# Performance work log

Measured on AMD Instinct MI355X. Metric: run time of the kernel, lower is better.

## Reference

```python
import jax, jax.numpy as jnp
import numpy as np
from jax import lax

EPS = 1e-5

# Straight-through identity binarization (torch code mutates .data, so autograd
# sees binarized values but grads flow as identity to the latent weights/inputs).
def ste_sign(x):
    return x + lax.stop_gradient(jnp.sign(x) - x)

# SignActivation: sign forward, hard-tanh-style gradient (zero where |i| > 1).
@jax.custom_vjp
def sign_act(x):
    return jnp.sign(x)

def _sa_fwd(x):
    return jnp.sign(x), x

def _sa_bwd(x, g):
    return (jnp.where(jnp.abs(x) <= 1.0, g, 0.0),)

sign_act.defvjp(_sa_fwd, _sa_bwd)

def bn2d(x, gamma, beta):
    # training-mode BatchNorm2d: batch stats over (N,H,W), biased variance
    mean = jnp.mean(x, axis=(0, 2, 3), keepdims=True)
    var = jnp.var(x, axis=(0, 2, 3), keepdims=True)
    xn = (x - mean) * lax.rsqrt(var + EPS)
    return xn * gamma.reshape(1, -1, 1, 1) + beta.reshape(1, -1, 1, 1)

def bn1d(x, gamma, beta):
    mean = jnp.mean(x, axis=0, keepdims=True)
    var = jnp.var(x, axis=0, keepdims=True)
    xn = (x - mean) * lax.rsqrt(var + EPS)
    return xn * gamma[None, :] + beta[None, :]

def conv2d(x, w, stride, pad):
    return lax.conv_general_dilated(
        x, w, window_strides=(stride, stride),
        padding=((pad, pad), (pad, pad)),
        dimension_numbers=("NCHW", "OIHW", "NCHW"))


def setup_inputs() -> dict:
    key = jax.random.key(0)
    ks = jax.random.split(key, 4)
    width = 0.01
    x = jax.random.normal(ks[0], (8192, 1, 28, 28), dtype=jnp.float32)
    w1 = jax.random.normal(ks[1], (32, 1, 5, 5), dtype=jnp.float32) * width
    w2 = jax.random.normal(ks[2], (64, 32, 4, 4), dtype=jnp.float32) * width
    w3 = jax.random.normal(ks[3], (10, 64 * 64), dtype=jnp.float32) * width
    g1 = jnp.ones((32,), jnp.float32); b1 = jnp.zeros((32,), jnp.float32)
    g2 = jnp.ones((64,), jnp.float32); b2 = jnp.zeros((64,), jnp.float32)
    g3 = jnp.ones((10,), jnp.float32); b3 = jnp.zeros((10,), jnp.float32)
    return {"x": x, "w1": w1, "g1": g1, "b1": b1,
            "w2": w2, "g2": g2, "b2": b2,
            "w3": w3, "g3": g3, "b3": b3}


def reference(x, w1, g1, b1, w2, g2, b2, w3, g3, b3):
    # cv1: input channels = 1 != 3 -> input binarized; weight binarized
    h = conv2d(ste_sign(x), ste_sign(w1), stride=2, pad=2)   # [B,32,14,14]
    h = bn2d(h, g1, b1)
    h = sign_act(h)
    # cv2: input channels 32 != 3 -> binarized (no-op on +-1 values)
    h = conv2d(ste_sign(h), ste_sign(w2), stride=2, pad=2)   # [B,64,8,8]
    h = bn2d(h, g2, b2)
    h = sign_act(h)
    h = h.reshape(h.shape[0], -1)                            # [B,4096]
    # fc3: features 4096 != 784 -> binarized (no-op on +-1 values)
    h = jnp.dot(ste_sign(h), ste_sign(w3).T)                 # [B,10]
    h = bn1d(h, g3, b3)
    return h
```

## Files before the change

kernel.cpp:

```cpp
#include <hip/hip_runtime.h>
#include <stdint.h>


#define NB 8192
typedef unsigned long long ull;

#define OFF_C1  ((size_t)0)
#define SZ_C1   ((size_t)NB*6272)
#define OFF_C2  (OFF_C1 + SZ_C1)
#define SZ_C2   ((size_t)NB*4096)
#define OFF_FC  (OFF_C2 + SZ_C2)
#define SZ_FC   ((size_t)NB*10*4)
#define OFF_S1  (OFF_FC + SZ_FC)
#define OFF_S2  (OFF_S1 + 2048)
#define OFF_S3  (OFF_S2 + 8192)
#define OFF_W2B (OFF_S3 + 2048)
#define OFF_W3B (OFF_W2B + 4096)

__device__ inline void mk_thresh(double s, double t, int &T, int &flip) {
    if (s > 0.0) {
        int v = (int)floor(-t / s) - 2;
        for (int c = 0; c < 6; ++c) { if (s * (double)v + t > 0.0) break; ++v; }
        T = v; flip = 0;
    } else if (s < 0.0) {
        int v = (int)floor(-t / s) - 2;
        for (int c = 0; c < 6; ++c) { if (!(s * (double)v + t > 0.0)) break; ++v; }
        T = v; flip = 1;
    } else { T = -200; flip = (t > 0.0) ? 0 : 1; }
}
__device__ inline int clampT(int T, int lim) {
    return (T < -lim) ? -lim : (T > lim) ? lim : T;
}

__global__ __launch_bounds__(256) void kA_conv1(
    const float* __restrict__ x, const float* __restrict__ w1,
    const float* __restrict__ w2, const float* __restrict__ w3,
    int8_t* __restrict__ c1out, int* __restrict__ stats1,
    ull* __restrict__ w2bT, ull* __restrict__ w3b)
{
    const int tid = threadIdx.x, lane = tid & 63, wv = tid >> 6;

    if (blockIdx.x == 2048) {
        for (int m = wv; m < 10; m += 4) {
            const float* wp = w3 + (size_t)m*4096;
            ull mine = 0ull;
            for (int ch = 0; ch < 64; ++ch) {
                const ull bal = __ballot(wp[(size_t)ch*64 + lane] > 0.f);
                if (lane == ch) mine = bal;
            }
            w3b[m*64 + lane] = mine;
        }
        for (int t = tid; t < 512; t += 256) {
            const int idx = t >> 6, k = t & 63;
            const int u = idx >> 1, pr = idx & 1;
            uint32_t lo = 0u, hi = 0u;
            for (int c = 0; c < 32; ++c) {
                const float* wp = w2 + (((k*32 + c)*4 + u)*4 + 2*pr);
                lo |= (wp[0] > 0.f ? 1u : 0u) << c;
                hi |= (wp[1] > 0.f ? 1u : 0u) << c;
            }
            w2bT[t] = (ull)lo | ((ull)hi << 32);
        }
        return;
    }

    __shared__ ull sxb[4][16];
    __shared__ uint32_t wfilt[32];
    __shared__ uint32_t outb[4][1568];
    __shared__ int lsum[32], lsq[32];

    if (tid < 32) {
        uint32_t f = 0u;
        #pragma unroll
        for (int q = 0; q < 25; ++q) f |= (w1[tid*25 + q] > 0.f ? 1u : 0u) << q;
        wfilt[tid] = f;
        lsum[tid] = 0; lsq[tid] = 0;
    }
    const int n = blockIdx.x*4 + wv;
    #pragma unroll
    for (int t = 0; t < 13; ++t) {
        const int idx = t*64 + lane;
        const float v = (idx < 784) ? x[(size_t)n*784 + idx] : -1.f;
        const ull bal = __ballot(v > 0.f);
        if (lane == t) sxb[wv][t] = bal;
    }
    if (lane == 13) sxb[wv][13] = 0ull;
    __syncthreads();
    for (int t = 0; t < 4; ++t) {
        const int p = t*64 + lane;
        if (p < 196) {
            const int i = p / 14, j = p - i*14;
            const uint32_t cmask = (j == 0) ? 0x1Cu : (j == 13) ? 0x0Fu : 0x1Fu;
            uint32_t win = 0u, vm = 0u;
            #pragma unroll
            for (int u = 0; u < 5; ++u) {
                const int r = 2*i + u - 2;
                if (r >= 0 && r < 28) {
                    const int bp = 28*r, w0 = bp >> 6, sh = bp & 63;
                    const ull a = sxb[wv][w0], b = sxb[wv][w0+1];
                    uint32_t row = (uint32_t)((a >> sh) | ((b << 1) << (63 - sh)));
                    row = (row & 0x0FFFFFFFu) << 2;
                    win |= ((row >> (2*j)) & 31u) << (5*u);
                    vm  |= cmask << (5*u);
                }
            }
            const int nv = __popc(vm);
            uint32_t dw[8];
            #pragma unroll
            for (int d = 0; d < 8; ++d) dw[d] = 0u;
            #pragma unroll
            for (int c = 0; c < 32; ++c) {
                const int diff = __popc((win ^ wfilt[c]) & vm);
                const int o = nv - 2*diff;
                dw[c >> 2] |= (uint32_t)(o & 255) << (8*(c & 3));
            }
            #pragma unroll
            for (int d = 0; d < 8; ++d) outb[wv][p*8 + d] = dw[d];
        }
    }
    __syncthreads();
    {
        int4* dst = (int4*)(c1out + (size_t)n*6272);
        const int4* src = (const int4*)&outb[wv][0];
        #pragma unroll
        for (int t = 0; t < 7; ++t) {
            const int idx = t*64 + lane;
            if (idx < 392) dst[idx] = src[idx];
        }
    }
    {
        const int ch = lane & 31, half = lane >> 5;
        const int8_t* ob = (const int8_t*)&outb[wv][0];
        int s = 0, q = 0;
        for (int p = half*98; p < half*98 + 98; ++p) {
            const int v = ob[p*32 + ch];
            s += v; q += v*v;
        }
        s += __shfl_xor(s, 32);
        q += __shfl_xor(q, 32);
        if (lane < 32) { atomicAdd(&lsum[lane], s); atomicAdd(&lsq[lane], q); }
    }
    __syncthreads();
    if (tid < 32) {
        const int shard = blockIdx.x & 7;
        atomicAdd(&stats1[(shard*32 + tid)*2 + 0], lsum[tid]);
        atomicAdd(&stats1[(shard*32 + tid)*2 + 1], lsq[tid]);
    }
}

__global__ __launch_bounds__(256) void kB_conv2(
    const int8_t* __restrict__ c1out, const int* __restrict__ stats1,
    const float* __restrict__ gm1, const float* __restrict__ bt1,
    const ull* __restrict__ w2bT,
    int8_t* __restrict__ c2out, ull* __restrict__ stats2)
{
    __shared__ ull BwU[4][14][8];
    __shared__ ull sW[512];
    __shared__ int sT1[32];
    __shared__ uint32_t sFlip1;
    __shared__ uint32_t cw[4][64][16];
    __shared__ int ssum[64], ssq[64];
    const int tid = threadIdx.x, lane = tid & 63, wv = tid >> 6;
    const int n0 = blockIdx.x * 4;

    for (int t = tid; t < 512; t += 256) sW[t] = w2bT[t];
    if (tid < 64) { ssum[tid] = 0; ssq[tid] = 0; }
    if (tid < 32) {
        long long s = 0, q = 0;
        for (int sh = 0; sh < 8; ++sh) {
            s += stats1[(sh*32 + tid)*2 + 0];
            q += stats1[(sh*32 + tid)*2 + 1];
        }
        const double N = 8192.0 * 196.0;
        const double mean = (double)s / N;
        const double var  = (double)q / N - mean*mean;
        const double a = (double)gm1[tid] / sqrt(var + 1e-5);
        const double b = (double)bt1[tid] - mean*a;
        int T, fl; mk_thresh(a, b, T, fl);
        sT1[tid] = clampT(T, 26);
        const ull bm = __ballot(fl != 0);
        if (tid == 0) sFlip1 = (uint32_t)bm;
    }
    __syncthreads();
    const uint32_t flipn1 = ~sFlip1;
    for (int t = tid; t < 784; t += 256) {
        const int im = t / 196, p = t - im*196;
        const int r = p / 14, c = p - r*14;
        const uint4* src = (const uint4*)(c1out + ((size_t)(n0+im)*196 + p)*32);
        const uint4 lo4 = src[0], hi4 = src[1];
        const uint32_t wsrc[8] = {lo4.x, lo4.y, lo4.z, lo4.w, hi4.x, hi4.y, hi4.z, hi4.w};
        uint32_t neg = 0u;
        #pragma unroll
        for (int d = 0; d < 8; ++d) {
            #pragma unroll
            for (int qq = 0; qq < 4; ++qq) {
                const int ch = d*4 + qq;
                const int v = (int)((int8_t)(wsrc[d] >> (8*qq)));
                neg |= ((uint32_t)(v - sT1[ch]) >> 31) << ch;
            }
        }
        ((uint32_t*)&BwU[im][r][0])[c] = neg ^ flipn1;
    }
    __syncthreads();
    ull W[8];
    #pragma unroll
    for (int idx = 0; idx < 8; ++idx) W[idx] = sW[idx*64 + lane];
    int s = 0, q = 0;
    #pragma unroll
    for (int i = 0; i < 8; ++i) {
        uint32_t packA = 0u;
        #pragma unroll
        for (int j = 0; j < 8; ++j) {
            int D = 0, nw = 0;
            #pragma unroll
            for (int u = 0; u < 4; ++u) {
                const int r = 2*i + u - 2;
                if (r < 0 || r > 13) continue;
                const ull* row = &BwU[wv][r][0];
                if (j >= 1) { D += __popcll(row[j-1] ^ W[2*u+0]); ++nw; }
                if (j <= 6) { D += __popcll(row[j]   ^ W[2*u+1]); ++nw; }
            }
            const int o = 32*nw - D;
            s += o; q += o*o;
            packA |= (uint32_t)(o & 255) << (8*(j & 3));
            if ((j & 3) == 3) { cw[wv][lane][2*i + (j >> 2)] = packA; packA = 0u; }
        }
    }
    atomicAdd(&ssum[lane], s);
    atomicAdd(&ssq[lane], q);
    __syncthreads();
    {
        const int n = n0 + wv;
        int4* dst = (int4*)(c2out + (size_t)n*4096);
        const int4* src = (const int4*)&cw[wv][0][0];
        #pragma unroll
        for (int t = 0; t < 4; ++t) dst[t*64 + lane] = src[t*64 + lane];
    }
    if (tid < 64) {
        const int shard = blockIdx.x & 7;
        atomicAdd(&stats2[(shard*64 + tid)*2 + 0], (ull)(long long)ssum[tid]);
        atomicAdd(&stats2[(shard*64 + tid)*2 + 1], (ull)(long long)ssq[tid]);
    }
}

__global__ __launch_bounds__(256) void kC_fc(
    const int8_t* __restrict__ c2o, const float* __restrict__ gm2,
    const float* __restrict__ bt2, const ull* __restrict__ stats2,
    const ull* __restrict__ w3b,
    int* __restrict__ fc, ull* __restrict__ stats3)
{
    __shared__ ull w3s[640];
    __shared__ int sT2[64];
    __shared__ ull sFlip2;
    __shared__ int fco[4][10];
    __shared__ int s3[10], q3[10];
    const int tid = threadIdx.x, lane = tid & 63, wv = tid >> 6;
    for (int t = tid; t < 640; t += 256) w3s[t] = w3b[t];
    if (tid < 10) { s3[tid] = 0; q3[tid] = 0; }
    if (tid < 64) {
        long long ss = 0, qq = 0;
        for (int sh = 0; sh < 8; ++sh) {
            ss += (long long)stats2[(sh*64 + tid)*2 + 0];
            qq += (long long)stats2[(sh*64 + tid)*2 + 1];
        }
        const double N = 8192.0 * 64.0;
        const double mh = (double)ss / N;
        const double vh = (double)qq / N - mh*mh;
        const double a = (double)gm2[tid] / sqrt(4.0*vh + 1e-5);
        const double b = (double)bt2[tid] - 2.0*mh*a;
        int T, fl; mk_thresh(2.0*a, b, T, fl);
        sT2[tid] = clampT(T, 200);
        const ull bm = __ballot(fl != 0);
        if (tid == 0) sFlip2 = bm;
    }
    __syncthreads();
    const int T2 = sT2[lane];
    const ull flipn2 = ~sFlip2;
    const int n = blockIdx.x*4 + wv;
    const uint4* src = (const uint4*)(c2o + (size_t)n*4096 + lane*64);
    uint32_t neglo = 0u, neghi = 0u;
    #pragma unroll
    for (int r4 = 0; r4 < 4; ++r4) {
        const uint4 v4 = src[r4];
        const uint32_t wsrc[4] = {v4.x, v4.y, v4.z, v4.w};
        #pragma unroll
        for (int c = 0; c < 4; ++c) {
            #pragma unroll
            for (int b = 0; b < 4; ++b) {
                const int p = r4*16 + c*4 + b;
                const int v = (int)((int8_t)(wsrc[c] >> (8*b)));
                const uint32_t bit = (uint32_t)(v - T2) >> 31;
                if (p < 32) neglo |= bit << p; else neghi |= bit << (p - 32);
            }
        }
    }
    const ull myw = ((ull)neglo | ((ull)neghi << 32)) ^ flipn2;
    uint32_t pk[5];
    #pragma unroll
    for (int t = 0; t < 5; ++t) {
        const uint32_t pa = (uint32_t)__popcll(myw ^ w3s[(2*t+0)*64 + lane]);
        const uint32_t pb = (uint32_t)__popcll(myw ^ w3s[(2*t+1)*64 + lane]);
        pk[t] = pa | (pb << 16);
    }
    #pragma unroll
    for (int off = 32; off >= 1; off >>= 1) {
        #pragma unroll
        for (int t = 0; t < 5; ++t) pk[t] += __shfl_xor(pk[t], off);
    }
    if (lane == 0) {
        #pragma unroll
        for (int m = 0; m < 10; ++m) {
            const int tot = (pk[m >> 1] >> (16*(m & 1))) & 0xFFFF;
            fco[wv][m] = 4096 - 2*tot;
        }
    }
    __syncthreads();
    if (tid < 40) {
        const int li = tid / 10, m = tid - li*10;
        const int o = fco[li][m];
        fc[(size_t)(blockIdx.x*4 + li)*10 + m] = o;
        atomicAdd(&s3[m], o);
        atomicAdd(&q3[m], o*o);
    }
    __syncthreads();
    if (tid < 10) {
        const int shard = blockIdx.x & 7;
        atomicAdd(&stats3[(shard*10 + tid)*2 + 0], (ull)(long long)s3[tid]);
        atomicAdd(&stats3[(shard*10 + tid)*2 + 1], (ull)(long long)q3[tid]);
    }
}

__global__ __launch_bounds__(256) void kD_apply(
    const int* __restrict__ fc, const float* __restrict__ gm3,
    const float* __restrict__ bt3, const ull* __restrict__ stats3,
    float* __restrict__ out)
{
    __shared__ float a3[10], b3[10];
    const int tid = threadIdx.x;
    if (tid < 10) {
        long long s = 0, q = 0;
        for (int sh = 0; sh < 8; ++sh) {
            s += (long long)stats3[(sh*10 + tid)*2 + 0];
            q += (long long)stats3[(sh*10 + tid)*2 + 1];
        }
        const double N = 8192.0;
        const double mean = (double)s / N;
        const double var  = (double)q / N - mean*mean;
        const double a = (double)gm3[tid] / sqrt(var + 1e-5);
        a3[tid] = (float)a;
        b3[tid] = (float)((double)bt3[tid] - mean*a);
    }
    __syncthreads();
    const int e = blockIdx.x*256 + tid;
    if (e < NB*10) {
        const int m = e % 10;
        out[e] = fmaf(a3[m], (float)fc[e], b3[m]);
    }
}

extern "C" void kernel_launch(void* const* d_in, const int* in_sizes, int n_in,
                              void* d_out, int out_size, void* d_ws, size_t ws_size,
                              hipStream_t stream)
{
    const float* x   = (const float*)d_in[0];
    const float* w1  = (const float*)d_in[1];
    const float* gm1 = (const float*)d_in[2];
    const float* bt1 = (const float*)d_in[3];
    const float* w2  = (const float*)d_in[4];
    const float* gm2 = (const float*)d_in[5];
    const float* bt2 = (const float*)d_in[6];
    const float* w3  = (const float*)d_in[7];
    const float* gm3 = (const float*)d_in[8];
    const float* bt3 = (const float*)d_in[9];
    char* ws = (char*)d_ws;
    int8_t* c1o = (int8_t*)(ws + OFF_C1);
    int8_t* c2o = (int8_t*)(ws + OFF_C2);
    int*    fcb = (int*)(ws + OFF_FC);
    int*    s1  = (int*)(ws + OFF_S1);
    ull*    s2  = (ull*)(ws + OFF_S2);
    ull*    s3  = (ull*)(ws + OFF_S3);
    ull*    w2bp = (ull*)(ws + OFF_W2B);
    ull*    w3bp = (ull*)(ws + OFF_W3B);

    hipMemsetAsync(ws + OFF_S1, 0, 12288, stream);
    kA_conv1<<<2049, 256, 0, stream>>>(x, w1, w2, w3, c1o, s1, w2bp, w3bp);
    kB_conv2<<<2048, 256, 0, stream>>>(c1o, s1, gm1, bt1, w2bp, c2o, s2);
    kC_fc   <<<2048, 256, 0, stream>>>(c2o, gm2, bt2, s2, w3bp, fcb, s3);
    kD_apply<<<320,  256, 0, stream>>>(fcb, gm3, bt3, s3, (float*)d_out);
}
```

Before: 184.6 us.

## Make conv and fc kernels per-wavefront independent, dropping block barriers and shared staging

```diff
diff --git a/kernel.cpp b/kernel.cpp
--- a/kernel.cpp
+++ b/kernel.cpp
@@ -76,6 +76,7 @@
         wfilt[tid] = f;
         lsum[tid] = 0; lsq[tid] = 0;
     }
+    __syncthreads();
     const int n = blockIdx.x*4 + wv;
     #pragma unroll
     for (int t = 0; t < 13; ++t) {
@@ -85,7 +86,6 @@
         if (lane == t) sxb[wv][t] = bal;
     }
     if (lane == 13) sxb[wv][13] = 0ull;
-    __syncthreads();
     for (int t = 0; t < 4; ++t) {
         const int p = t*64 + lane;
         if (p < 196) {
@@ -118,7 +118,6 @@
             for (int d = 0; d < 8; ++d) outb[wv][p*8 + d] = dw[d];
         }
     }
-    __syncthreads();
     {
         int4* dst = (int4*)(c1out + (size_t)n*6272);
         const int4* src = (const int4*)&outb[wv][0];
@@ -155,38 +154,38 @@
     int8_t* __restrict__ c2out, ull* __restrict__ stats2)
 {
     __shared__ ull BwU[4][14][8];
-    __shared__ ull sW[512];
-    __shared__ int sT1[32];
-    __shared__ uint32_t sFlip1;
-    __shared__ uint32_t cw[4][64][16];
+    __shared__ int sT1[4][32];
+    __shared__ uint32_t cw[4][64][17];
     __shared__ int ssum[64], ssq[64];
     const int tid = threadIdx.x, lane = tid & 63, wv = tid >> 6;
-    const int n0 = blockIdx.x * 4;
-
-    for (int t = tid; t < 512; t += 256) sW[t] = w2bT[t];
+    const int n = blockIdx.x*4 + wv;
+
+    ull W[8];
+    #pragma unroll
+    for (int idx = 0; idx < 8; ++idx) W[idx] = w2bT[idx*64 + lane];
+
     if (tid < 64) { ssum[tid] = 0; ssq[tid] = 0; }
-    if (tid < 32) {
+    int fl = 0;
+    if (lane < 32) {
         long long s = 0, q = 0;
         for (int sh = 0; sh < 8; ++sh) {
-            s += stats1[(sh*32 + tid)*2 + 0];
-            q += stats1[(sh*32 + tid)*2 + 1];
+            s += stats1[(sh*32 + lane)*2 + 0];
+            q += stats1[(sh*32 + lane)*2 + 1];
         }
         const double N = 8192.0 * 196.0;
         const double mean = (double)s / N;
         const double var  = (double)q / N - mean*mean;
-        const double a = (double)gm1[tid] / sqrt(var + 1e-5);
-        const double b = (double)bt1[tid] - mean*a;
-        int T, fl; mk_thresh(a, b, T, fl);
-        sT1[tid] = clampT(T, 26);
-        const ull bm = __ballot(fl != 0);
-        if (tid == 0) sFlip1 = (uint32_t)bm;
-    }
-    __syncthreads();
-    const uint32_t flipn1 = ~sFlip1;
-    for (int t = tid; t < 784; t += 256) {
-        const int im = t / 196, p = t - im*196;
-        const int r = p / 14, c = p - r*14;
-        const uint4* src = (const uint4*)(c1out + ((size_t)(n0+im)*196 + p)*32);
+        const double a = (double)gm1[lane] / sqrt(var + 1e-5);
+        const double b = (double)bt1[lane] - mean*a;
+        int T; mk_thresh(a, b, T, fl);
+        sT1[wv][lane] = clampT(T, 26);
+    }
+    const uint32_t flipn1 = ~(uint32_t)__ballot(fl != 0);
+    __syncthreads();
+
+    for (int t = lane; t < 196; t += 64) {
+        const int r = t / 14, c = t - r*14;
+        const uint4* src = (const uint4*)(c1out + ((size_t)n*196 + t)*32);
         const uint4 lo4 = src[0], hi4 = src[1];
         const uint32_t wsrc[8] = {lo4.x, lo4.y, lo4.z, lo4.w, hi4.x, hi4.y, hi4.z, hi4.w};
         uint32_t neg = 0u;
@@ -196,15 +195,11 @@
             for (int qq = 0; qq < 4; ++qq) {
                 const int ch = d*4 + qq;
                 const int v = (int)((int8_t)(wsrc[d] >> (8*qq)));
-                neg |= ((uint32_t)(v - sT1[ch]) >> 31) << ch;
-            }
-        }
-        ((uint32_t*)&BwU[im][r][0])[c] = neg ^ flipn1;
-    }
-    __syncthreads();
-    ull W[8];
-    #pragma unroll
-    for (int idx = 0; idx < 8; ++idx) W[idx] = sW[idx*64 + lane];
+                neg |= ((uint32_t)(v - sT1[wv][ch]) >> 31) << ch;
+            }
+        }
+        ((uint32_t*)&BwU[wv][r][0])[c] = neg ^ flipn1;
+    }
     int s = 0, q = 0;
     #pragma unroll
     for (int i = 0; i < 8; ++i) {
@@ -228,14 +223,15 @@
     }
     atomicAdd(&ssum[lane], s);
     atomicAdd(&ssq[lane], q);
-    __syncthreads();
     {
-        const int n = n0 + wv;
-        int4* dst = (int4*)(c2out + (size_t)n*4096);
-        const int4* src = (const int4*)&cw[wv][0][0];
-        #pragma unroll
-        for (int t = 0; t < 4; ++t) dst[t*64 + lane] = src[t*64 + lane];
-    }
+        uint32_t* dst = (uint32_t*)(c2out + (size_t)n*4096);
+        #pragma unroll
+        for (int t = 0; t < 16; ++t) {
+            const int g = t*64 + lane;
+            dst[g] = cw[wv][g >> 4][g & 15];
+        }
+    }
+    __syncthreads();
     if (tid < 64) {
         const int shard = blockIdx.x & 7;
         atomicAdd(&stats2[(shard*64 + tid)*2 + 0], (ull)(long long)ssum[tid]);
@@ -249,33 +245,26 @@
     const ull* __restrict__ w3b,
     int* __restrict__ fc, ull* __restrict__ stats3)
 {
-    __shared__ ull w3s[640];
-    __shared__ int sT2[64];
-    __shared__ ull sFlip2;
     __shared__ int fco[4][10];
     __shared__ int s3[10], q3[10];
     const int tid = threadIdx.x, lane = tid & 63, wv = tid >> 6;
-    for (int t = tid; t < 640; t += 256) w3s[t] = w3b[t];
     if (tid < 10) { s3[tid] = 0; q3[tid] = 0; }
-    if (tid < 64) {
+    int T2, fl;
+    {
         long long ss = 0, qq = 0;
         for (int sh = 0; sh < 8; ++sh) {
-            ss += (long long)stats2[(sh*64 + tid)*2 + 0];
-            qq += (long long)stats2[(sh*64 + tid)*2 + 1];
+            ss += (long long)stats2[(sh*64 + lane)*2 + 0];
+            qq += (long long)stats2[(sh*64 + lane)*2 + 1];
         }
         const double N = 8192.0 * 64.0;
         const double mh = (double)ss / N;
         const double vh = (double)qq / N - mh*mh;
-        const double a = (double)gm2[tid] / sqrt(4.0*vh + 1e-5);
-        const double b = (double)bt2[tid] - 2.0*mh*a;
-        int T, fl; mk_thresh(2.0*a, b, T, fl);
-        sT2[tid] = clampT(T, 200);
-        const ull bm = __ballot(fl != 0);
-        if (tid == 0) sFlip2 = bm;
-    }
-    __syncthreads();
-    const int T2 = sT2[lane];
-    const ull flipn2 = ~sFlip2;
+        const double a = (double)gm2[lane] / sqrt(4.0*vh + 1e-5);
+        const double b = (double)bt2[lane] - 2.0*mh*a;
+        int T; mk_thresh(2.0*a, b, T, fl);
+        T2 = clampT(T, 200);
+    }
+    const ull flipn2 = ~__ballot(fl != 0);
     const int n = blockIdx.x*4 + wv;
     const uint4* src = (const uint4*)(c2o + (size_t)n*4096 + lane*64);
     uint32_t neglo = 0u, neghi = 0u;
@@ -298,8 +287,8 @@
     uint32_t pk[5];
     #pragma unroll
     for (int t = 0; t < 5; ++t) {
-        const uint32_t pa = (uint32_t)__popcll(myw ^ w3s[(2*t+0)*64 + lane]);
-        const uint32_t pb = (uint32_t)__popcll(myw ^ w3s[(2*t+1)*64 + lane]);
+        const uint32_t pa = (uint32_t)__popcll(myw ^ w3b[(2*t+0)*64 + lane]);
+        const uint32_t pb = (uint32_t)__popcll(myw ^ w3b[(2*t+1)*64 + lane]);
         pk[t] = pa | (pb << 16);
     }
     #pragma unroll
```

After: 181.6 us. Within noise of the previous version (-1.6%).
